# Optimization experiments

Hardware: AMD Instinct MI355X
Metric: run time of the kernel (lower is better)

Reference implementation:

```python
import jax, jax.numpy as jnp
import numpy as np
import math

D = 256
H = 8
HD = D // H
FF = 1024


def pos2posemb(pos, num_pos_feats=64, temperature=10000.0):
    scale = 2 * math.pi
    pos = pos * scale
    dim_t = jnp.arange(num_pos_feats, dtype=jnp.float32)
    dim_t = temperature ** (2.0 * jnp.floor(dim_t / 2) / num_pos_feats)
    pe = pos[..., None] / dim_t  # [N,4,64]
    pe = jnp.stack((jnp.sin(pe[..., 0::2]), jnp.cos(pe[..., 1::2])), axis=-1)  # [N,4,32,2]
    return pe.reshape(pe.shape[0], -1)  # [N,256]


def layer_norm(x, w, b, eps=1e-5):
    m = jnp.mean(x, axis=-1, keepdims=True)
    v = jnp.mean((x - m) ** 2, axis=-1, keepdims=True)
    return (x - m) * jax.lax.rsqrt(v + eps) * w + b


def setup_inputs() -> dict:
    key = jax.random.key(0)
    ks = jax.random.split(key, 24)
    N = 4096
    s = 0.02
    inp = {
        "ref_pts": jax.random.uniform(ks[0], (N, 4), jnp.float32),
        "pred_boxes": jax.random.uniform(ks[1], (N, 4), jnp.float32),
        "scores": jax.random.uniform(ks[2], (N,), jnp.float32),
        "output_embedding": jax.random.normal(ks[3], (N, D), jnp.float32),
        "query_pos": jax.random.normal(ks[4], (N, D), jnp.float32),
        "group_ids": jax.random.randint(ks[5], (N,), 0, 4, jnp.int64),
        "g_size": 4,
        "in_proj_w": jax.random.normal(ks[6], (3 * D, D), jnp.float32) * s,
        "in_proj_b": jnp.zeros((3 * D,), jnp.float32),
        "out_proj_w": jax.random.normal(ks[7], (D, D), jnp.float32) * s,
        "out_proj_b": jnp.zeros((D,), jnp.float32),
        "lin1_w": jax.random.normal(ks[8], (FF, D), jnp.float32) * s,
        "lin1_b": jnp.zeros((FF,), jnp.float32),
        "lin2_w": jax.random.normal(ks[9], (D, FF), jnp.float32) * s,
        "lin2_b": jnp.zeros((D,), jnp.float32),
        "feat1_w": jax.random.normal(ks[10], (FF, D), jnp.float32) * s,
        "feat1_b": jnp.zeros((FF,), jnp.float32),
        "feat2_w": jax.random.normal(ks[11], (D, FF), jnp.float32) * s,
        "feat2_b": jnp.zeros((D,), jnp.float32),
        "norm1_w": jnp.ones((D,), jnp.float32),
        "norm1_b": jnp.zeros((D,), jnp.float32),
        "norm2_w": jnp.ones((D,), jnp.float32),
        "norm2_b": jnp.zeros((D,), jnp.float32),
        "normf_w": jnp.ones((D,), jnp.float32),
        "normf_b": jnp.zeros((D,), jnp.float32),
    }
    return inp


def reference(ref_pts, pred_boxes, scores, output_embedding, query_pos,
              in_proj_w, in_proj_b, out_proj_w, out_proj_b,
              lin1_w, lin1_b, lin2_w, lin2_b,
              feat1_w, feat1_b, feat2_w, feat2_b,
              norm1_w, norm1_b, norm2_w, norm2_b, normf_w, normf_b,
              group_ids, g_size):
    N = ref_pts.shape[0]
    is_pos = scores > 0.5  # score_thr = 0.5
    # ref_pts[is_pos] = pred_boxes.detach()[is_pos]
    ref = jnp.where(is_pos[:, None], jax.lax.stop_gradient(pred_boxes), ref_pts)

    out_embed = output_embedding
    qpos_emb = pos2posemb(ref)  # [N,256]
    qk = qpos_emb + out_embed

    # grouped block-diagonal mask: 0 within same group, -inf across groups
    mask = jnp.where(group_ids[:, None] == group_ids[None, :], 0.0, -jnp.inf)

    # MultiheadAttention (eval, dropout=0)
    q = qk @ in_proj_w[:D].T + in_proj_b[:D]
    k = qk @ in_proj_w[D:2 * D].T + in_proj_b[D:2 * D]
    v = out_embed @ in_proj_w[2 * D:].T + in_proj_b[2 * D:]
    qh = q.reshape(N, H, HD)
    kh = k.reshape(N, H, HD)
    vh = v.reshape(N, H, HD)
    logits = jnp.einsum("nhd,mhd->hnm", qh, kh) / jnp.sqrt(jnp.float32(HD)) + mask
    attn = jax.nn.softmax(logits, axis=-1)
    ctx = jnp.einsum("hnm,mhd->nhd", attn, vh).reshape(N, D)
    tgt2 = ctx @ out_proj_w.T + out_proj_b

    tgt = layer_norm(out_embed + tgt2, norm1_w, norm1_b)
    ffn = jax.nn.relu(tgt @ lin1_w.T + lin1_b) @ lin2_w.T + lin2_b
    tgt = layer_norm(tgt + ffn, norm2_w, norm2_b)

    feat = jax.nn.relu(tgt @ feat1_w.T + feat1_b) @ feat2_w.T + feat2_b
    query_feat = layer_norm(query_pos + feat, normf_w, normf_b)

    # query_pos[is_pos] = query_feat[is_pos]
    query_pos_out = jnp.where(is_pos[:, None], query_feat, query_pos)
    return query_pos_out
```

## Files before the change

kernel.cpp:

```cpp
#include <hip/hip_runtime.h>


typedef __attribute__((ext_vector_type(8))) __bf16 bf16x8;
typedef __attribute__((ext_vector_type(4))) float f32x4;

#define NSPLIT 2

static __device__ __forceinline__ unsigned short f2bf(float f) {
    union { float f; unsigned u; } v; v.f = f;
    unsigned r = v.u + 0x7fffu + ((v.u >> 16) & 1u);
    return (unsigned short)(r >> 16);
}

__global__ __launch_bounds__(1024) void k_setup(
    const float* __restrict__ w0, const float* __restrict__ w1,
    const float* __restrict__ w2, const float* __restrict__ w3,
    const float* __restrict__ w4, const float* __restrict__ w5,
    unsigned short* __restrict__ o0, unsigned short* __restrict__ o1,
    unsigned short* __restrict__ o2, unsigned short* __restrict__ o3,
    unsigned short* __restrict__ o4, unsigned short* __restrict__ o5,
    const int* __restrict__ gid, int N,
    int* __restrict__ perm, int* __restrict__ rank,
    int* __restrict__ gid_s, int* __restrict__ offs)
{
    if (blockIdx.x < 320) {
        long i = ((long)blockIdx.x * 1024 + threadIdx.x) * 4;
        const float* src; unsigned short* dst; long off;
        if      (i <  196608) { src = w0; dst = o0; off = i; }
        else if (i <  262144) { src = w1; dst = o1; off = i -  196608; }
        else if (i <  524288) { src = w2; dst = o2; off = i -  262144; }
        else if (i <  786432) { src = w3; dst = o3; off = i -  524288; }
        else if (i < 1048576) { src = w4; dst = o4; off = i -  786432; }
        else                  { src = w5; dst = o5; off = i - 1048576; }
        float4 v = *(const float4*)(src + off);
        ushort4 o; o.x = f2bf(v.x); o.y = f2bf(v.y); o.z = f2bf(v.z); o.w = f2bf(v.w);
        *(ushort4*)(dst + off) = o;
        return;
    }
    __shared__ int cnt[1024][4];
    __shared__ int base[4];
    int t = threadIdx.x;
    int per = N / 1024;
    int c[4] = {0, 0, 0, 0};
    for (int i = 0; i < per; ++i) c[gid[t * per + i] & 3]++;
    for (int g = 0; g < 4; ++g) cnt[t][g] = c[g];
    __syncthreads();
    for (int off = 1; off < 1024; off <<= 1) {
        int v[4] = {0, 0, 0, 0};
        if (t >= off) for (int g = 0; g < 4; ++g) v[g] = cnt[t - off][g];
        __syncthreads();
        if (t >= off) for (int g = 0; g < 4; ++g) cnt[t][g] += v[g];
        __syncthreads();
    }
    if (t == 0) {
        base[0] = 0;
        base[1] = cnt[1023][0];
        base[2] = base[1] + cnt[1023][1];
        base[3] = base[2] + cnt[1023][2];
        offs[0] = 0; offs[1] = base[1]; offs[2] = base[2]; offs[3] = base[3]; offs[4] = N;
    }
    __syncthreads();
    int run[4];
    for (int g = 0; g < 4; ++g) run[g] = base[g] + (t ? cnt[t - 1][g] : 0);
    for (int i = 0; i < per; ++i) {
        int n = t * per + i;
        int g = gid[n] & 3;
        int p = run[g]++;
        perm[p] = n; rank[n] = p; gid_s[p] = g;
    }
}

__global__ __launch_bounds__(256) void k_prep(
    const float* __restrict__ ref_pts, const float* __restrict__ pred_boxes,
    const float* __restrict__ scores, const float* __restrict__ embed,
    const float* __restrict__ qpos, const int* __restrict__ rank,
    unsigned short* __restrict__ qk_bf, unsigned short* __restrict__ emb_bf,
    float* __restrict__ emb_f32s, float* __restrict__ qpos_s,
    float* __restrict__ scores_s)
{
    int n = blockIdx.x, d = threadIdx.x;
    int pos = rank[n];
    bool ip = scores[n] > 0.5f;
    int c = d >> 6, k = (d >> 1) & 31, s = d & 1;
    float p = (ip ? pred_boxes : ref_pts)[n * 4 + c] * 6.283185307179586f;
    float freq = exp2f(-(float)k * (13.287712379549449f / 32.0f));
    float ang = p * freq;
    float e = s ? cosf(ang) : sinf(ang);
    float em = embed[(size_t)n * 256 + d];
    qk_bf[(size_t)pos * 256 + d] = f2bf(e + em);
    emb_bf[(size_t)pos * 256 + d] = f2bf(em);
    emb_f32s[(size_t)pos * 256 + d] = em;
    qpos_s[(size_t)pos * 256 + d] = qpos[(size_t)n * 256 + d];
    if (d == 0) scores_s[pos] = scores[n];
}

#define EPI_QKV     0
#define EPI_RELUBF  3

template<int EPI>
__global__ __launch_bounds__(256) void k_gemm(
    const unsigned short* __restrict__ A, const unsigned short* __restrict__ A2,
    const unsigned short* __restrict__ B,
    const float* __restrict__ bias,
    void* __restrict__ out, void* __restrict__ out2,
    int M, int Nout, int K)
{
    __shared__ __align__(16) unsigned short As[2][64][72];
    __shared__ __align__(16) unsigned short Bs[2][64][72];
    int mt = M >> 6;
    int bm = blockIdx.x % mt, bn = blockIdx.x / mt;
    int m0 = bm * 64, c0 = bn * 64;
    int tid = threadIdx.x;
    int wave = tid >> 6, lane = tid & 63;
    int wr = wave >> 1, wc = wave & 1;
    int g = lane >> 4, r15 = lane & 15;

    const unsigned short* Asrc = A;
    if constexpr (EPI == EPI_QKV) { if (c0 >= 512) Asrc = A2; }

    int r0 = tid >> 3, u0 = tid & 7;
    int r1 = 32 + (tid >> 3), u1 = tid & 7;

    const unsigned short* Abase = Asrc + (size_t)m0 * K;
    const unsigned short* Bbase = B + (size_t)c0 * K;

    uint4 a0 = *(const uint4*)(Abase + (size_t)r0 * K + u0 * 8);
    uint4 a1 = *(const uint4*)(Abase + (size_t)r1 * K + u1 * 8);
    uint4 b0 = *(const uint4*)(Bbase + (size_t)r0 * K + u0 * 8);
    uint4 b1 = *(const uint4*)(Bbase + (size_t)r1 * K + u1 * 8);
    *(uint4*)(&As[0][r0][u0 * 8]) = a0;
    *(uint4*)(&As[0][r1][u1 * 8]) = a1;
    *(uint4*)(&Bs[0][r0][u0 * 8]) = b0;
    *(uint4*)(&Bs[0][r1][u1 * 8]) = b1;
    __syncthreads();

    f32x4 acc[2][2] = {};
    int nk = K >> 6;
    for (int kt = 0; kt < nk; ++kt) {
        int cur = kt & 1;
        bool more = (kt + 1 < nk);
        if (more) {
            int kc = (kt + 1) << 6;
            a0 = *(const uint4*)(Abase + (size_t)r0 * K + kc + u0 * 8);
            a1 = *(const uint4*)(Abase + (size_t)r1 * K + kc + u1 * 8);
            b0 = *(const uint4*)(Bbase + (size_t)r0 * K + kc + u0 * 8);
            b1 = *(const uint4*)(Bbase + (size_t)r1 * K + kc + u1 * 8);
        }
        #pragma unroll
        for (int kk = 0; kk < 2; ++kk) {
            bf16x8 af0 = *(const bf16x8*)(&As[cur][wr * 32 + r15][kk * 32 + g * 8]);
            bf16x8 af1 = *(const bf16x8*)(&As[cur][wr * 32 + 16 + r15][kk * 32 + g * 8]);
            bf16x8 bf0 = *(const bf16x8*)(&Bs[cur][wc * 32 + r15][kk * 32 + g * 8]);
            bf16x8 bf1 = *(const bf16x8*)(&Bs[cur][wc * 32 + 16 + r15][kk * 32 + g * 8]);
            acc[0][0] = __builtin_amdgcn_mfma_f32_16x16x32_bf16(af0, bf0, acc[0][0], 0, 0, 0);
            acc[0][1] = __builtin_amdgcn_mfma_f32_16x16x32_bf16(af0, bf1, acc[0][1], 0, 0, 0);
            acc[1][0] = __builtin_amdgcn_mfma_f32_16x16x32_bf16(af1, bf0, acc[1][0], 0, 0, 0);
            acc[1][1] = __builtin_amdgcn_mfma_f32_16x16x32_bf16(af1, bf1, acc[1][1], 0, 0, 0);
        }
        if (more) {
            *(uint4*)(&As[cur ^ 1][r0][u0 * 8]) = a0;
            *(uint4*)(&As[cur ^ 1][r1][u1 * 8]) = a1;
            *(uint4*)(&Bs[cur ^ 1][r0][u0 * 8]) = b0;
            *(uint4*)(&Bs[cur ^ 1][r1][u1 * 8]) = b1;
            __syncthreads();
        }
    }

    #pragma unroll
    for (int ti = 0; ti < 2; ++ti)
    #pragma unroll
    for (int tj = 0; tj < 2; ++tj)
    #pragma unroll
    for (int r = 0; r < 4; ++r) {
        int n = m0 + wr * 32 + ti * 16 + g * 4 + r;
        int o = c0 + wc * 32 + tj * 16 + r15;
        float v = acc[ti][tj][r] + bias[o];
        if constexpr (EPI == EPI_QKV) {
            if (o < 512) {
                float s = (o < 256) ? (0.17677669529663687f * 1.4426950408889634f) : 1.0f;
                ((unsigned short*)out)[(size_t)n * 512 + o] = f2bf(v * s);
            } else {
                ((unsigned short*)out2)[(size_t)(o - 512) * M + n] = f2bf(v);
            }
        } else {
            ((unsigned short*)out)[(size_t)n * Nout + o] = f2bf(fmaxf(v, 0.0f));
        }
    }
}

template<int K, int MODE>
__global__ __launch_bounds__(256) void k_gemmln(
    const unsigned short* __restrict__ Abf,
    const float* __restrict__ Opart, const float* __restrict__ lpart,
    const unsigned short* __restrict__ Bw,
    const float* __restrict__ bias, const float* __restrict__ resid,
    const float* __restrict__ lnw, const float* __restrict__ lnb,
    float* __restrict__ outf32, unsigned short* __restrict__ outbf,
    const float* __restrict__ scores_s, const int* __restrict__ perm, int N)
{
    __shared__ __align__(16) unsigned short As[2][16][72];
    __shared__ float sW[4][16];
    __shared__ float qW[4][16];
    __shared__ float mS[16], rS[16];

    const int m0 = blockIdx.x * 16;
    const int tid = threadIdx.x, wave = tid >> 6, lane = tid & 63;
    const int g = lane >> 4, r15 = lane & 15;

    const int ar = tid >> 3, au = tid & 7;
    const bool stager = (tid < 128);

    auto loadA = [&](int kt) -> uint4 {
        int n = m0 + ar;
        int c = kt * 64 + au * 8;
        if constexpr (MODE == 0) {
            int h = c >> 5;
            float l0 = lpart[(size_t)n * 8 + h];
            float l1 = lpart[((size_t)N + n) * 8 + h];
            float inv = 1.0f / (l0 + l1);
            const float* p0 = Opart + (size_t)n * 256 + c;
            const float* p1 = Opart + ((size_t)N + n) * 256 + c;
            float4 x0 = *(const float4*)(p0);
            float4 x1 = *(const float4*)(p0 + 4);
            float4 y0 = *(const float4*)(p1);
            float4 y1 = *(const float4*)(p1 + 4);
            uint4 o;
            o.x = f2bf((x0.x + y0.x) * inv) | ((unsigned)f2bf((x0.y + y0.y) * inv) << 16);
            o.y = f2bf((x0.z + y0.z) * inv) | ((unsigned)f2bf((x0.w + y0.w) * inv) << 16);
            o.z = f2bf((x1.x + y1.x) * inv) | ((unsigned)f2bf((x1.y + y1.y) * inv) << 16);
            o.w = f2bf((x1.z + y1.z) * inv) | ((unsigned)f2bf((x1.w + y1.w) * inv) << 16);
            return o;
        } else {
            return *(const uint4*)(Abf + (size_t)n * K + c);
        }
    };

    const unsigned short* Bb = Bw + (size_t)(wave * 64 + r15) * K + g * 8;
#define LOADB(dst, kt, kk, tj) dst = *(const bf16x8*)(Bb + (size_t)(tj) * 16 * K + (kt) * 64 + (kk) * 32)

    bf16x8 c00, c01, c02, c03, c10, c11, c12, c13;
    uint4 pa;
    if (stager) { pa = loadA(0); *(uint4*)(&As[0][ar][au * 8]) = pa; }
    LOADB(c00, 0, 0, 0); LOADB(c01, 0, 0, 1); LOADB(c02, 0, 0, 2); LOADB(c03, 0, 0, 3);
    LOADB(c10, 0, 1, 0); LOADB(c11, 0, 1, 1); LOADB(c12, 0, 1, 2); LOADB(c13, 0, 1, 3);
    __syncthreads();

    f32x4 acc[4] = {};
    constexpr int nk = K >> 6;
    for (int kt = 0; kt < nk; ++kt) {
        int cur = kt & 1;
        bool more = (kt + 1 < nk);
        bf16x8 n00, n01, n02, n03, n10, n11, n12, n13;
        if (more) {
            if (stager) pa = loadA(kt + 1);
            LOADB(n00, kt + 1, 0, 0); LOADB(n01, kt + 1, 0, 1);
            LOADB(n02, kt + 1, 0, 2); LOADB(n03, kt + 1, 0, 3);
            LOADB(n10, kt + 1, 1, 0); LOADB(n11, kt + 1, 1, 1);
            LOADB(n12, kt + 1, 1, 2); LOADB(n13, kt + 1, 1, 3);
        }
        bf16x8 af0 = *(const bf16x8*)(&As[cur][r15][g * 8]);
        acc[0] = __builtin_amdgcn_mfma_f32_16x16x32_bf16(af0, c00, acc[0], 0, 0, 0);
        acc[1] = __builtin_amdgcn_mfma_f32_16x16x32_bf16(af0, c01, acc[1], 0, 0, 0);
        acc[2] = __builtin_amdgcn_mfma_f32_16x16x32_bf16(af0, c02, acc[2], 0, 0, 0);
        acc[3] = __builtin_amdgcn_mfma_f32_16x16x32_bf16(af0, c03, acc[3], 0, 0, 0);
        bf16x8 af1 = *(const bf16x8*)(&As[cur][r15][32 + g * 8]);
        acc[0] = __builtin_amdgcn_mfma_f32_16x16x32_bf16(af1, c10, acc[0], 0, 0, 0);
        acc[1] = __builtin_amdgcn_mfma_f32_16x16x32_bf16(af1, c11, acc[1], 0, 0, 0);
        acc[2] = __builtin_amdgcn_mfma_f32_16x16x32_bf16(af1, c12, acc[2], 0, 0, 0);
        acc[3] = __builtin_amdgcn_mfma_f32_16x16x32_bf16(af1, c13, acc[3], 0, 0, 0);
        if (more) {
            if (stager) *(uint4*)(&As[cur ^ 1][ar][au * 8]) = pa;
            __syncthreads();
            c00 = n00; c01 = n01; c02 = n02; c03 = n03;
            c10 = n10; c11 = n11; c12 = n12; c13 = n13;
        }
    }
#undef LOADB

    float vals[4][4];
    float vs[4] = {0.f, 0.f, 0.f, 0.f}, vq[4] = {0.f, 0.f, 0.f, 0.f};
    #pragma unroll
    for (int tj = 0; tj < 4; ++tj) {
        int col = wave * 64 + tj * 16 + r15;
        float b = bias[col];
        #pragma unroll
        for (int r = 0; r < 4; ++r) {
            int row = g * 4 + r;
            float v = acc[tj][r] + b + resid[(size_t)(m0 + row) * 256 + col];
            vals[tj][r] = v;
            vs[r] += v; vq[r] += v * v;
        }
    }
    #pragma unroll
    for (int off = 1; off < 16; off <<= 1)
        #pragma unroll
        for (int r = 0; r < 4; ++r) {
            vs[r] += __shfl_xor(vs[r], off, 64);
            vq[r] += __shfl_xor(vq[r], off, 64);
        }
    if (r15 == 0) {
        #pragma unroll
        for (int r = 0; r < 4; ++r) { sW[wave][g * 4 + r] = vs[r]; qW[wave][g * 4 + r] = vq[r]; }
    }
    __syncthreads();
    if (tid < 16) {
        float s = sW[0][tid] + sW[1][tid] + sW[2][tid] + sW[3][tid];
        float q = qW[0][tid] + qW[1][tid] + qW[2][tid] + qW[3][tid];
        float mean = s * (1.0f / 256.0f);
        float var = q * (1.0f / 256.0f) - mean * mean;
        mS[tid] = mean;
        rS[tid] = rsqrtf(fmaxf(var, 0.f) + 1e-5f);
    }
    __syncthreads();

    #pragma unroll
    for (int tj = 0; tj < 4; ++tj) {
        int col = wave * 64 + tj * 16 + r15;
        float w = lnw[col], bb = lnb[col];
        #pragma unroll
        for (int r = 0; r < 4; ++r) {
            int row = g * 4 + r;
            float o = (vals[tj][r] - mS[row]) * rS[row] * w + bb;
            if constexpr (MODE == 0) {
                outf32[(size_t)(m0 + row) * 256 + col] = o;
                outbf[(size_t)(m0 + row) * 256 + col] = f2bf(o);
            } else if constexpr (MODE == 1) {
                outbf[(size_t)(m0 + row) * 256 + col] = f2bf(o);
            } else {
                bool ip = scores_s[m0 + row] > 0.5f;
                float qp = resid[(size_t)(m0 + row) * 256 + col];
                int no = perm[m0 + row];
                outf32[(size_t)no * 256 + col] = ip ? o : qp;
            }
        }
    }
}

__global__ __launch_bounds__(256) void k_attn(
    const unsigned short* __restrict__ QK, const unsigned short* __restrict__ Vt,
    const int* __restrict__ gid_s, const int* __restrict__ offs,
    float* __restrict__ Opart, float* __restrict__ lpart, int N)
{
    __shared__ __align__(16) unsigned short Ks[2][64][40];
    __shared__ __align__(16) unsigned short Vs[2][32][72];
    __shared__ __align__(16) unsigned short Ps[4][16][64];
    __shared__ __align__(16) int gks[2][64];

    int qtiles = N >> 6;
    int bid = blockIdx.x;
    int qt = bid % qtiles;
    int hs = bid / qtiles;
    int h = hs & 7;
    int sp = hs >> 3;
    int q0 = qt * 64;
    int tid = threadIdx.x, wave = tid >> 6, lane = tid & 63;
    int g = lane >> 4, r15 = lane & 15;
    int n0 = q0 + wave * 16;

    int g_lo = gid_s[q0], g_hi = gid_s[q0 + 63];
    int tlo = offs[g_lo] >> 6;
    int thi = (offs[g_hi + 1] + 63) >> 6;
    int ntiles = thi - tlo;
    int chunk = (ntiles + NSPLIT - 1) / NSPLIT;
    int t0 = tlo + sp * chunk;
    int t1 = min(t0 + chunk, thi);

    if (t0 >= t1) {
        #pragma unroll
        for (int r = 0; r < 4; ++r) {
            int n = n0 + g * 4 + r;
            Opart[((size_t)sp * N + n) * 256 + h * 32 + r15] = 0.f;
            Opart[((size_t)sp * N + n) * 256 + h * 32 + 16 + r15] = 0.f;
        }
        if (g == 0) lpart[((size_t)sp * N + n0 + r15) * 8 + h] = 0.f;
        return;
    }

    bf16x8 qf = *(const bf16x8*)(QK + (size_t)(n0 + r15) * 512 + h * 32 + g * 8);
    int gq = gid_s[n0 + r15];

    int kr_ = tid >> 2, kc_ = (tid & 3) * 8;
    int vd_ = tid >> 3, vc_ = (tid & 7) * 8;

    f32x4 O0 = {}, O1 = {};
    float lloc = 0.f;
    unsigned short* PsW = &Ps[wave][0][0];

    {
        int m0 = t0 << 6;
        *(uint4*)(&Ks[0][kr_][kc_]) = *(const uint4*)(QK + (size_t)(m0 + kr_) * 512 + 256 + h * 32 + kc_);
        *(uint4*)(&Vs[0][vd_][vc_]) = *(const uint4*)(Vt + (size_t)(h * 32 + vd_) * N + m0 + vc_);
        if (tid < 64) gks[0][tid] = gid_s[m0 + tid];
    }
    __syncthreads();

    int cur = 0;
    for (int t = t0; t < t1; ++t) {
        bool more = (t + 1 < t1);
        uint4 kn, vn; int gn = 0;
        if (more) {
            int m0n = (t + 1) << 6;
            kn = *(const uint4*)(QK + (size_t)(m0n + kr_) * 512 + 256 + h * 32 + kc_);
            vn = *(const uint4*)(Vt + (size_t)(h * 32 + vd_) * N + m0n + vc_);
            if (tid < 64) gn = gid_s[m0n + tid];
        }

        f32x4 S[4];
        #pragma unroll
        for (int t_ = 0; t_ < 4; ++t_) {
            bf16x8 kf = *(const bf16x8*)(&Ks[cur][t_ * 16 + r15][g * 8]);
            f32x4 z = {};
            S[t_] = __builtin_amdgcn_mfma_f32_16x16x32_bf16(kf, qf, z, 0, 0, 0);
        }
        #pragma unroll
        for (int t_ = 0; t_ < 4; ++t_) {
            int4 g4 = *(const int4*)(&gks[cur][t_ * 16 + g * 4]);
            float p0 = (g4.x == gq) ? exp2f(S[t_][0]) : 0.f;
            float p1 = (g4.y == gq) ? exp2f(S[t_][1]) : 0.f;
            float p2 = (g4.z == gq) ? exp2f(S[t_][2]) : 0.f;
            float p3 = (g4.w == gq) ? exp2f(S[t_][3]) : 0.f;
            lloc += (p0 + p1) + (p2 + p3);
            ushort4 pw;
            pw.x = f2bf(p0); pw.y = f2bf(p1); pw.z = f2bf(p2); pw.w = f2bf(p3);
            int off = t_ * 32 + g * 8;
            int byte = r15 * 128 + ((((off >> 4) ^ (r15 & 7)) << 4) | (off & 15));
            *(ushort4*)((char*)PsW + byte) = pw;
        }
        #pragma unroll
        for (int kk = 0; kk < 2; ++kk) {
            int byte = r15 * 128 + (((kk * 4 + g) ^ (r15 & 7)) << 4);
            bf16x8 pf = *(const bf16x8*)((char*)PsW + byte);
            bf16x8 v0 = *(const bf16x8*)(&Vs[cur][r15][kk * 32 + g * 8]);
            bf16x8 v1 = *(const bf16x8*)(&Vs[cur][16 + r15][kk * 32 + g * 8]);
            O0 = __builtin_amdgcn_mfma_f32_16x16x32_bf16(pf, v0, O0, 0, 0, 0);
            O1 = __builtin_amdgcn_mfma_f32_16x16x32_bf16(pf, v1, O1, 0, 0, 0);
        }

        if (more) {
            *(uint4*)(&Ks[cur ^ 1][kr_][kc_]) = kn;
            *(uint4*)(&Vs[cur ^ 1][vd_][vc_]) = vn;
            if (tid < 64) gks[cur ^ 1][tid] = gn;
        }
        __syncthreads();
        cur ^= 1;
    }

    float l = lloc;
    l += __shfl_xor(l, 16, 64);
    l += __shfl_xor(l, 32, 64);
    if (g == 0) lpart[((size_t)sp * N + n0 + r15) * 8 + h] = l;

    #pragma unroll
    for (int r = 0; r < 4; ++r) {
        int n = n0 + g * 4 + r;
        Opart[((size_t)sp * N + n) * 256 + h * 32 + r15]      = O0[r];
        Opart[((size_t)sp * N + n) * 256 + h * 32 + 16 + r15] = O1[r];
    }
}

extern "C" void kernel_launch(void* const* d_in, const int* in_sizes, int n_in,
                              void* d_out, int out_size, void* d_ws, size_t ws_size,
                              hipStream_t stream)
{
    const float* ref_pts    = (const float*)d_in[0];
    const float* pred_boxes = (const float*)d_in[1];
    const float* scores     = (const float*)d_in[2];
    const float* out_embed  = (const float*)d_in[3];
    const float* query_pos  = (const float*)d_in[4];
    const int*   group_ids  = (const int*)d_in[5];
    const float* in_proj_w  = (const float*)d_in[7];
    const float* in_proj_b  = (const float*)d_in[8];
    const float* out_proj_w = (const float*)d_in[9];
    const float* out_proj_b = (const float*)d_in[10];
    const float* lin1_w     = (const float*)d_in[11];
    const float* lin1_b     = (const float*)d_in[12];
    const float* lin2_w     = (const float*)d_in[13];
    const float* lin2_b     = (const float*)d_in[14];
    const float* feat1_w    = (const float*)d_in[15];
    const float* feat1_b    = (const float*)d_in[16];
    const float* feat2_w    = (const float*)d_in[17];
    const float* feat2_b    = (const float*)d_in[18];
    const float* norm1_w    = (const float*)d_in[19];
    const float* norm1_b    = (const float*)d_in[20];
    const float* norm2_w    = (const float*)d_in[21];
    const float* norm2_b    = (const float*)d_in[22];
    const float* normf_w    = (const float*)d_in[23];
    const float* normf_b    = (const float*)d_in[24];

    const int N = in_sizes[2];

    char* ws = (char*)d_ws;
    size_t off = 0;
    auto alloc = [&](size_t bytes) -> void* {
        void* p = ws + off; off += (bytes + 255) & ~(size_t)255; return p;
    };
    unsigned short* wqkv   = (unsigned short*)alloc((size_t)768 * 256 * 2);
    unsigned short* wout   = (unsigned short*)alloc((size_t)256 * 256 * 2);
    unsigned short* wlin1  = (unsigned short*)alloc((size_t)1024 * 256 * 2);
    unsigned short* wlin2  = (unsigned short*)alloc((size_t)256 * 1024 * 2);
    unsigned short* wfeat1 = (unsigned short*)alloc((size_t)1024 * 256 * 2);
    unsigned short* wfeat2 = (unsigned short*)alloc((size_t)256 * 1024 * 2);
    unsigned short* qk_bf  = (unsigned short*)alloc((size_t)N * 256 * 2);
    unsigned short* emb_bf = (unsigned short*)alloc((size_t)N * 256 * 2);
    unsigned short* QKbuf  = (unsigned short*)alloc((size_t)N * 512 * 2);
    unsigned short* Vtbuf  = (unsigned short*)alloc((size_t)256 * N * 2);
    float*          tgtf   = (float*)alloc((size_t)N * 256 * 4);
    unsigned short* tgtbf  = (unsigned short*)alloc((size_t)N * 256 * 2);
    unsigned short* t2bf   = (unsigned short*)alloc((size_t)N * 256 * 2);
    unsigned short* hbuf   = (unsigned short*)alloc((size_t)N * 1024 * 2);
    float* emb_f32s = (float*)alloc((size_t)N * 256 * 4);
    float* qpos_s   = (float*)alloc((size_t)N * 256 * 4);
    float* scores_s = (float*)alloc((size_t)N * 4);
    int* permbuf = (int*)alloc((size_t)N * 4);
    int* rankbuf = (int*)alloc((size_t)N * 4);
    int* gidsbuf = (int*)alloc((size_t)N * 4);
    int* offsbuf = (int*)alloc(32 * 4);
    float* Opartbuf = (float*)alloc((size_t)NSPLIT * N * 256 * 4);
    float* lbuf     = (float*)alloc((size_t)NSPLIT * N * 8 * 4);
    (void)ws_size; (void)n_in; (void)out_size;

    const int mt = N >> 6;

    k_setup<<<321, 1024, 0, stream>>>(in_proj_w, out_proj_w, lin1_w, lin2_w, feat1_w, feat2_w,
                                      wqkv, wout, wlin1, wlin2, wfeat1, wfeat2,
                                      group_ids, N, permbuf, rankbuf, gidsbuf, offsbuf);
    k_prep<<<N, 256, 0, stream>>>(ref_pts, pred_boxes, scores, out_embed, query_pos, rankbuf,
                                  qk_bf, emb_bf, emb_f32s, qpos_s, scores_s);
    k_gemm<EPI_QKV><<<mt * 12, 256, 0, stream>>>(
        qk_bf, emb_bf, wqkv, in_proj_b, QKbuf, Vtbuf, N, 768, 256);
    k_attn<<<mt * 8 * NSPLIT, 256, 0, stream>>>(QKbuf, Vtbuf, gidsbuf, offsbuf,
                                                Opartbuf, lbuf, N);
    k_gemmln<256, 0><<<N / 16, 256, 0, stream>>>(
        nullptr, Opartbuf, lbuf, wout, out_proj_b, emb_f32s,
        norm1_w, norm1_b, tgtf, tgtbf, nullptr, nullptr, N);
    k_gemm<EPI_RELUBF><<<mt * 16, 256, 0, stream>>>(
        tgtbf, nullptr, wlin1, lin1_b, hbuf, nullptr, N, 1024, 256);
    k_gemmln<1024, 1><<<N / 16, 256, 0, stream>>>(
        hbuf, nullptr, nullptr, wlin2, lin2_b, tgtf,
        norm2_w, norm2_b, nullptr, t2bf, nullptr, nullptr, N);
    k_gemm<EPI_RELUBF><<<mt * 16, 256, 0, stream>>>(
        t2bf, nullptr, wfeat1, feat1_b, hbuf, nullptr, N, 1024, 256);
    k_gemmln<1024, 2><<<N / 16, 256, 0, stream>>>(
        hbuf, nullptr, nullptr, wfeat2, feat2_b, qpos_s,
        normf_w, normf_b, (float*)d_out, nullptr, scores_s, permbuf, N);
}
```

Baseline: 123.4 us.

## Fuse FFN up-projection, ReLU, down-projection and LayerNorm into one kernel

Each of the two FFN stages (lin1/lin2 and feat1/feat2) now runs as a single 512-thread kernel per 16-row tile. It computes the 1024-wide ReLU hidden activation into shared memory, then does the down-projection, residual add and LayerNorm without a global round trip. This removes the N×1024 bf16 hidden buffer write and read-back and two kernel launches per FFN. In exchange, the fused kernel uses 16-row tiles, so each block re-streams the full W1 and W2 weights from cache, and its larger LDS footprint may limit occupancy.

```diff
diff --git a/kernel.cpp b/kernel.cpp
--- a/kernel.cpp
+++ b/kernel.cpp
@@ -94,8 +94,7 @@
     if (d == 0) scores_s[pos] = scores[n];
 }
 
-#define EPI_QKV     0
-#define EPI_RELUBF  3
+#define EPI_QKV 0
 
 template<int EPI>
 __global__ __launch_bounds__(256) void k_gemm(
@@ -175,28 +174,21 @@
         int n = m0 + wr * 32 + ti * 16 + g * 4 + r;
         int o = c0 + wc * 32 + tj * 16 + r15;
         float v = acc[ti][tj][r] + bias[o];
-        if constexpr (EPI == EPI_QKV) {
-            if (o < 512) {
-                float s = (o < 256) ? (0.17677669529663687f * 1.4426950408889634f) : 1.0f;
-                ((unsigned short*)out)[(size_t)n * 512 + o] = f2bf(v * s);
-            } else {
-                ((unsigned short*)out2)[(size_t)(o - 512) * M + n] = f2bf(v);
-            }
+        if (o < 512) {
+            float s = (o < 256) ? (0.17677669529663687f * 1.4426950408889634f) : 1.0f;
+            ((unsigned short*)out)[(size_t)n * 512 + o] = f2bf(v * s);
         } else {
-            ((unsigned short*)out)[(size_t)n * Nout + o] = f2bf(fmaxf(v, 0.0f));
-        }
-    }
-}
-
-template<int K, int MODE>
-__global__ __launch_bounds__(256) void k_gemmln(
-    const unsigned short* __restrict__ Abf,
+            ((unsigned short*)out2)[(size_t)(o - 512) * M + n] = f2bf(v);
+        }
+    }
+}
+
+__global__ __launch_bounds__(256) void k_gemmln0(
     const float* __restrict__ Opart, const float* __restrict__ lpart,
     const unsigned short* __restrict__ Bw,
     const float* __restrict__ bias, const float* __restrict__ resid,
     const float* __restrict__ lnw, const float* __restrict__ lnb,
-    float* __restrict__ outf32, unsigned short* __restrict__ outbf,
-    const float* __restrict__ scores_s, const int* __restrict__ perm, int N)
+    float* __restrict__ outf32, unsigned short* __restrict__ outbf, int N)
 {
     __shared__ __align__(16) unsigned short As[2][16][72];
     __shared__ float sW[4][16];
@@ -206,37 +198,32 @@
     const int m0 = blockIdx.x * 16;
     const int tid = threadIdx.x, wave = tid >> 6, lane = tid & 63;
     const int g = lane >> 4, r15 = lane & 15;
-
     const int ar = tid >> 3, au = tid & 7;
     const bool stager = (tid < 128);
 
     auto loadA = [&](int kt) -> uint4 {
         int n = m0 + ar;
         int c = kt * 64 + au * 8;
-        if constexpr (MODE == 0) {
-            int h = c >> 5;
-            float l0 = lpart[(size_t)n * 8 + h];
-            float l1 = lpart[((size_t)N + n) * 8 + h];
-            float inv = 1.0f / (l0 + l1);
-            const float* p0 = Opart + (size_t)n * 256 + c;
-            const float* p1 = Opart + ((size_t)N + n) * 256 + c;
-            float4 x0 = *(const float4*)(p0);
-            float4 x1 = *(const float4*)(p0 + 4);
-            float4 y0 = *(const float4*)(p1);
-            float4 y1 = *(const float4*)(p1 + 4);
-            uint4 o;
-            o.x = f2bf((x0.x + y0.x) * inv) | ((unsigned)f2bf((x0.y + y0.y) * inv) << 16);
-            o.y = f2bf((x0.z + y0.z) * inv) | ((unsigned)f2bf((x0.w + y0.w) * inv) << 16);
-            o.z = f2bf((x1.x + y1.x) * inv) | ((unsigned)f2bf((x1.y + y1.y) * inv) << 16);
-            o.w = f2bf((x1.z + y1.z) * inv) | ((unsigned)f2bf((x1.w + y1.w) * inv) << 16);
-            return o;
-        } else {
-            return *(const uint4*)(Abf + (size_t)n * K + c);
-        }
+        int h = c >> 5;
+        float l0 = lpart[(size_t)n * 8 + h];
+        float l1 = lpart[((size_t)N + n) * 8 + h];
+        float inv = 1.0f / (l0 + l1);
+        const float* p0 = Opart + (size_t)n * 256 + c;
+        const float* p1 = Opart + ((size_t)N + n) * 256 + c;
+        float4 x0 = *(const float4*)(p0);
+        float4 x1 = *(const float4*)(p0 + 4);
+        float4 y0 = *(const float4*)(p1);
+        float4 y1 = *(const float4*)(p1 + 4);
+        uint4 o;
+        o.x = f2bf((x0.x + y0.x) * inv) | ((unsigned)f2bf((x0.y + y0.y) * inv) << 16);
+        o.y = f2bf((x0.z + y0.z) * inv) | ((unsigned)f2bf((x0.w + y0.w) * inv) << 16);
+        o.z = f2bf((x1.x + y1.x) * inv) | ((unsigned)f2bf((x1.y + y1.y) * inv) << 16);
+        o.w = f2bf((x1.z + y1.z) * inv) | ((unsigned)f2bf((x1.w + y1.w) * inv) << 16);
+        return o;
     };
 
-    const unsigned short* Bb = Bw + (size_t)(wave * 64 + r15) * K + g * 8;
-#define LOADB(dst, kt, kk, tj) dst = *(const bf16x8*)(Bb + (size_t)(tj) * 16 * K + (kt) * 64 + (kk) * 32)
+    const unsigned short* Bb = Bw + (size_t)(wave * 64 + r15) * 256 + g * 8;
+#define LOADB(dst, kt, kk, tj) dst = *(const bf16x8*)(Bb + (size_t)(tj) * 16 * 256 + (kt) * 64 + (kk) * 32)
 
     bf16x8 c00, c01, c02, c03, c10, c11, c12, c13;
     uint4 pa;
@@ -246,10 +233,10 @@
     __syncthreads();
 
     f32x4 acc[4] = {};
-    constexpr int nk = K >> 6;
-    for (int kt = 0; kt < nk; ++kt) {
+    #pragma unroll
+    for (int kt = 0; kt < 4; ++kt) {
         int cur = kt & 1;
-        bool more = (kt + 1 < nk);
+        bool more = (kt + 1 < 4);
         bf16x8 n00, n01, n02, n03, n10, n11, n12, n13;
         if (more) {
             if (stager) pa = loadA(kt + 1);
@@ -321,10 +308,165 @@
         for (int r = 0; r < 4; ++r) {
             int row = g * 4 + r;
             float o = (vals[tj][r] - mS[row]) * rS[row] * w + bb;
-            if constexpr (MODE == 0) {
-                outf32[(size_t)(m0 + row) * 256 + col] = o;
-                outbf[(size_t)(m0 + row) * 256 + col] = f2bf(o);
-            } else if constexpr (MODE == 1) {
+            outf32[(size_t)(m0 + row) * 256 + col] = o;
+            outbf[(size_t)(m0 + row) * 256 + col] = f2bf(o);
+        }
+    }
+}
+
+template<int MODE>
+__global__ __launch_bounds__(512) void k_ffn(
+    const unsigned short* __restrict__ Abf,
+    const unsigned short* __restrict__ W1, const float* __restrict__ b1,
+    const unsigned short* __restrict__ W2, const float* __restrict__ b2,
+    const float* __restrict__ resid,
+    const float* __restrict__ lnw, const float* __restrict__ lnb,
+    float* __restrict__ outf32, unsigned short* __restrict__ outbf,
+    const float* __restrict__ scores_s, const int* __restrict__ perm, int N)
+{
+    __shared__ __align__(16) unsigned short Xs[16][264];
+    __shared__ __align__(16) unsigned short Hs[16][1032];
+    __shared__ float sW[8][16];
+    __shared__ float qW[8][16];
+    __shared__ float mS[16], rS[16];
+
+    const int m0 = blockIdx.x * 16;
+    const int tid = threadIdx.x, wave = tid >> 6, lane = tid & 63;
+    const int g = lane >> 4, r15 = lane & 15;
+
+    {
+        int row = tid >> 5, ch = tid & 31;
+        *(uint4*)(&Xs[row][ch * 8]) = *(const uint4*)(Abf + (size_t)(m0 + row) * 256 + ch * 8);
+    }
+    __syncthreads();
+
+    const unsigned short* B1b = W1 + (size_t)(wave * 128 + r15) * 256 + g * 8;
+#define LB1(dst, ob, kt, kk, tj) \
+    dst = *(const bf16x8*)(B1b + (size_t)((ob) * 64 + (tj) * 16) * 256 + (kt) * 64 + (kk) * 32)
+
+    {
+        bf16x8 bc[8], bn[8];
+        LB1(bc[0], 0, 0, 0, 0); LB1(bc[1], 0, 0, 0, 1); LB1(bc[2], 0, 0, 0, 2); LB1(bc[3], 0, 0, 0, 3);
+        LB1(bc[4], 0, 0, 1, 0); LB1(bc[5], 0, 0, 1, 1); LB1(bc[6], 0, 0, 1, 2); LB1(bc[7], 0, 0, 1, 3);
+        #pragma unroll
+        for (int ob = 0; ob < 2; ++ob) {
+            f32x4 acc[4] = {};
+            #pragma unroll
+            for (int kt = 0; kt < 4; ++kt) {
+                bool more = (ob * 4 + kt + 1 < 8);
+                if (more) {
+                    int s = ob * 4 + kt + 1;
+                    int obn = s >> 2, ktn = s & 3;
+                    LB1(bn[0], obn, ktn, 0, 0); LB1(bn[1], obn, ktn, 0, 1);
+                    LB1(bn[2], obn, ktn, 0, 2); LB1(bn[3], obn, ktn, 0, 3);
+                    LB1(bn[4], obn, ktn, 1, 0); LB1(bn[5], obn, ktn, 1, 1);
+                    LB1(bn[6], obn, ktn, 1, 2); LB1(bn[7], obn, ktn, 1, 3);
+                }
+                bf16x8 a0 = *(const bf16x8*)(&Xs[r15][kt * 64 + g * 8]);
+                acc[0] = __builtin_amdgcn_mfma_f32_16x16x32_bf16(a0, bc[0], acc[0], 0, 0, 0);
+                acc[1] = __builtin_amdgcn_mfma_f32_16x16x32_bf16(a0, bc[1], acc[1], 0, 0, 0);
+                acc[2] = __builtin_amdgcn_mfma_f32_16x16x32_bf16(a0, bc[2], acc[2], 0, 0, 0);
+                acc[3] = __builtin_amdgcn_mfma_f32_16x16x32_bf16(a0, bc[3], acc[3], 0, 0, 0);
+                bf16x8 a1 = *(const bf16x8*)(&Xs[r15][kt * 64 + 32 + g * 8]);
+                acc[0] = __builtin_amdgcn_mfma_f32_16x16x32_bf16(a1, bc[4], acc[0], 0, 0, 0);
+                acc[1] = __builtin_amdgcn_mfma_f32_16x16x32_bf16(a1, bc[5], acc[1], 0, 0, 0);
+                acc[2] = __builtin_amdgcn_mfma_f32_16x16x32_bf16(a1, bc[6], acc[2], 0, 0, 0);
+                acc[3] = __builtin_amdgcn_mfma_f32_16x16x32_bf16(a1, bc[7], acc[3], 0, 0, 0);
+                if (more) {
+                    #pragma unroll
+                    for (int i = 0; i < 8; ++i) bc[i] = bn[i];
+                }
+            }
+            #pragma unroll
+            for (int tj = 0; tj < 4; ++tj) {
+                int col = wave * 128 + ob * 64 + tj * 16 + r15;
+                float b = b1[col];
+                #pragma unroll
+                for (int r = 0; r < 4; ++r) {
+                    Hs[g * 4 + r][col] = f2bf(fmaxf(acc[tj][r] + b, 0.0f));
+                }
+            }
+        }
+    }
+#undef LB1
+    __syncthreads();
+
+    const unsigned short* B2b = W2 + (size_t)(wave * 32 + r15) * 1024 + g * 8;
+#define LB2(dst, kt, kk, tj) \
+    dst = *(const bf16x8*)(B2b + (size_t)(tj) * 16 * 1024 + (kt) * 64 + (kk) * 32)
+
+    f32x4 acc2[2] = {};
+    {
+        bf16x8 bc[4], bn[4];
+        LB2(bc[0], 0, 0, 0); LB2(bc[1], 0, 0, 1);
+        LB2(bc[2], 0, 1, 0); LB2(bc[3], 0, 1, 1);
+        #pragma unroll
+        for (int kt = 0; kt < 16; ++kt) {
+            bool more = (kt + 1 < 16);
+            if (more) {
+                LB2(bn[0], kt + 1, 0, 0); LB2(bn[1], kt + 1, 0, 1);
+                LB2(bn[2], kt + 1, 1, 0); LB2(bn[3], kt + 1, 1, 1);
+            }
+            bf16x8 a0 = *(const bf16x8*)(&Hs[r15][kt * 64 + g * 8]);
+            acc2[0] = __builtin_amdgcn_mfma_f32_16x16x32_bf16(a0, bc[0], acc2[0], 0, 0, 0);
+            acc2[1] = __builtin_amdgcn_mfma_f32_16x16x32_bf16(a0, bc[1], acc2[1], 0, 0, 0);
+            bf16x8 a1 = *(const bf16x8*)(&Hs[r15][kt * 64 + 32 + g * 8]);
+            acc2[0] = __builtin_amdgcn_mfma_f32_16x16x32_bf16(a1, bc[2], acc2[0], 0, 0, 0);
+            acc2[1] = __builtin_amdgcn_mfma_f32_16x16x32_bf16(a1, bc[3], acc2[1], 0, 0, 0);
+            if (more) {
+                #pragma unroll
+                for (int i = 0; i < 4; ++i) bc[i] = bn[i];
+            }
+        }
+    }
+#undef LB2
+
+    float vals[2][4];
+    float vs[4] = {0.f, 0.f, 0.f, 0.f}, vq[4] = {0.f, 0.f, 0.f, 0.f};
+    #pragma unroll
+    for (int tj = 0; tj < 2; ++tj) {
+        int col = wave * 32 + tj * 16 + r15;
+        float b = b2[col];
+        #pragma unroll
+        for (int r = 0; r < 4; ++r) {
+            int row = g * 4 + r;
+            float v = acc2[tj][r] + b + resid[(size_t)(m0 + row) * 256 + col];
+            vals[tj][r] = v;
+            vs[r] += v; vq[r] += v * v;
+        }
+    }
+    #pragma unroll
+    for (int off = 1; off < 16; off <<= 1)
+        #pragma unroll
+        for (int r = 0; r < 4; ++r) {
+            vs[r] += __shfl_xor(vs[r], off, 64);
+            vq[r] += __shfl_xor(vq[r], off, 64);
+        }
+    if (r15 == 0) {
+        #pragma unroll
+        for (int r = 0; r < 4; ++r) { sW[wave][g * 4 + r] = vs[r]; qW[wave][g * 4 + r] = vq[r]; }
+    }
+    __syncthreads();
+    if (tid < 16) {
+        float s = 0.f, q = 0.f;
+        #pragma unroll
+        for (int w = 0; w < 8; ++w) { s += sW[w][tid]; q += qW[w][tid]; }
+        float mean = s * (1.0f / 256.0f);
+        float var = q * (1.0f / 256.0f) - mean * mean;
+        mS[tid] = mean;
+        rS[tid] = rsqrtf(fmaxf(var, 0.f) + 1e-5f);
+    }
+    __syncthreads();
+
+    #pragma unroll
+    for (int tj = 0; tj < 2; ++tj) {
+        int col = wave * 32 + tj * 16 + r15;
+        float w = lnw[col], bb = lnb[col];
+        #pragma unroll
+        for (int r = 0; r < 4; ++r) {
+            int row = g * 4 + r;
+            float o = (vals[tj][r] - mS[row]) * rS[row] * w + bb;
+            if constexpr (MODE == 1) {
                 outbf[(size_t)(m0 + row) * 256 + col] = f2bf(o);
             } else {
                 bool ip = scores_s[m0 + row] > 0.5f;
@@ -507,7 +649,6 @@
     float*          tgtf   = (float*)alloc((size_t)N * 256 * 4);
     unsigned short* tgtbf  = (unsigned short*)alloc((size_t)N * 256 * 2);
     unsigned short* t2bf   = (unsigned short*)alloc((size_t)N * 256 * 2);
-    unsigned short* hbuf   = (unsigned short*)alloc((size_t)N * 1024 * 2);
     float* emb_f32s = (float*)alloc((size_t)N * 256 * 4);
     float* qpos_s   = (float*)alloc((size_t)N * 256 * 4);
     float* scores_s = (float*)alloc((size_t)N * 4);
@@ -530,17 +671,13 @@
         qk_bf, emb_bf, wqkv, in_proj_b, QKbuf, Vtbuf, N, 768, 256);
     k_attn<<<mt * 8 * NSPLIT, 256, 0, stream>>>(QKbuf, Vtbuf, gidsbuf, offsbuf,
                                                 Opartbuf, lbuf, N);
-    k_gemmln<256, 0><<<N / 16, 256, 0, stream>>>(
-        nullptr, Opartbuf, lbuf, wout, out_proj_b, emb_f32s,
-        norm1_w, norm1_b, tgtf, tgtbf, nullptr, nullptr, N);
-    k_gemm<EPI_RELUBF><<<mt * 16, 256, 0, stream>>>(
-        tgtbf, nullptr, wlin1, lin1_b, hbuf, nullptr, N, 1024, 256);
-    k_gemmln<1024, 1><<<N / 16, 256, 0, stream>>>(
-        hbuf, nullptr, nullptr, wlin2, lin2_b, tgtf,
+    k_gemmln0<<<N / 16, 256, 0, stream>>>(
+        Opartbuf, lbuf, wout, out_proj_b, emb_f32s,
+        norm1_w, norm1_b, tgtf, tgtbf, N);
+    k_ffn<1><<<N / 16, 512, 0, stream>>>(
+        tgtbf, wlin1, lin1_b, wlin2, lin2_b, tgtf,
         norm2_w, norm2_b, nullptr, t2bf, nullptr, nullptr, N);
-    k_gemm<EPI_RELUBF><<<mt * 16, 256, 0, stream>>>(
-        t2bf, nullptr, wfeat1, feat1_b, hbuf, nullptr, N, 1024, 256);
-    k_gemmln<1024, 2><<<N / 16, 256, 0, stream>>>(
-        hbuf, nullptr, nullptr, wfeat2, feat2_b, qpos_s,
+    k_ffn<2><<<N / 16, 512, 0, stream>>>(
+        t2bf, wfeat1, feat1_b, wfeat2, feat2_b, qpos_s,
         normf_w, normf_b, (float*)d_out, nullptr, scores_s, permbuf, N);
 }
```

Result: slower. 135.5 us (+9.8%).

## Fuse prep into setup kernel, gather permuted rows in GEMMs, raise attention split

Applied to the files above, without the earlier changes.

Merges the per-row preprocessing into the setup launch, so it runs alongside the weight conversion and sort. Rows are no longer scattered into sorted order; instead the QKV GEMM and the LN epilogues gather through the permutation. This removes the sorted copies of the fp32 embedding, query_pos and scores, along with one kernel launch. Attention split-K goes from 2 to 4 and the merge step loops over the splits, which adds more partial-output traffic. The gemmln K loop is also fully unrolled.

```diff
diff --git a/kernel.cpp b/kernel.cpp
--- a/kernel.cpp
+++ b/kernel.cpp
@@ -4,7 +4,7 @@
 typedef __attribute__((ext_vector_type(8))) __bf16 bf16x8;
 typedef __attribute__((ext_vector_type(4))) float f32x4;
 
-#define NSPLIT 2
+#define NSPLIT 4
 
 static __device__ __forceinline__ unsigned short f2bf(float f) {
     union { float f; unsigned u; } v; v.f = f;
@@ -20,11 +20,14 @@
     unsigned short* __restrict__ o2, unsigned short* __restrict__ o3,
     unsigned short* __restrict__ o4, unsigned short* __restrict__ o5,
     const int* __restrict__ gid, int N,
-    int* __restrict__ perm, int* __restrict__ rank,
-    int* __restrict__ gid_s, int* __restrict__ offs)
+    int* __restrict__ perm, int* __restrict__ gid_s, int* __restrict__ offs,
+    const float* __restrict__ ref_pts, const float* __restrict__ pred_boxes,
+    const float* __restrict__ scores, const float* __restrict__ embed,
+    unsigned short* __restrict__ qk_bf, unsigned short* __restrict__ emb_bf)
 {
-    if (blockIdx.x < 320) {
-        long i = ((long)blockIdx.x * 1024 + threadIdx.x) * 4;
+    int bid = blockIdx.x, tid = threadIdx.x;
+    if (bid < 320) {
+        long i = ((long)bid * 1024 + tid) * 4;
         const float* src; unsigned short* dst; long off;
         if      (i <  196608) { src = w0; dst = o0; off = i; }
         else if (i <  262144) { src = w1; dst = o1; off = i -  196608; }
@@ -37,49 +40,41 @@
         *(ushort4*)(dst + off) = o;
         return;
     }
-    __shared__ int cnt[1024][4];
-    __shared__ int base[4];
-    int t = threadIdx.x;
-    int per = N / 1024;
-    int c[4] = {0, 0, 0, 0};
-    for (int i = 0; i < per; ++i) c[gid[t * per + i] & 3]++;
-    for (int g = 0; g < 4; ++g) cnt[t][g] = c[g];
-    __syncthreads();
-    for (int off = 1; off < 1024; off <<= 1) {
-        int v[4] = {0, 0, 0, 0};
-        if (t >= off) for (int g = 0; g < 4; ++g) v[g] = cnt[t - off][g];
+    if (bid == 320) {
+        __shared__ int cnt[1024][4];
+        __shared__ int base[4];
+        int t = tid;
+        int per = N / 1024;
+        int c[4] = {0, 0, 0, 0};
+        for (int i = 0; i < per; ++i) c[gid[t * per + i] & 3]++;
+        for (int g = 0; g < 4; ++g) cnt[t][g] = c[g];
         __syncthreads();
-        if (t >= off) for (int g = 0; g < 4; ++g) cnt[t][g] += v[g];
+        for (int off = 1; off < 1024; off <<= 1) {
+            int v[4] = {0, 0, 0, 0};
+            if (t >= off) for (int g = 0; g < 4; ++g) v[g] = cnt[t - off][g];
+            __syncthreads();
+            if (t >= off) for (int g = 0; g < 4; ++g) cnt[t][g] += v[g];
+            __syncthreads();
+        }
+        if (t == 0) {
+            base[0] = 0;
+            base[1] = cnt[1023][0];
+            base[2] = base[1] + cnt[1023][1];
+            base[3] = base[2] + cnt[1023][2];
+            offs[0] = 0; offs[1] = base[1]; offs[2] = base[2]; offs[3] = base[3]; offs[4] = N;
+        }
         __syncthreads();
-    }
-    if (t == 0) {
-        base[0] = 0;
-        base[1] = cnt[1023][0];
-        base[2] = base[1] + cnt[1023][1];
-        base[3] = base[2] + cnt[1023][2];
-        offs[0] = 0; offs[1] = base[1]; offs[2] = base[2]; offs[3] = base[3]; offs[4] = N;
-    }
-    __syncthreads();
-    int run[4];
-    for (int g = 0; g < 4; ++g) run[g] = base[g] + (t ? cnt[t - 1][g] : 0);
-    for (int i = 0; i < per; ++i) {
-        int n = t * per + i;
-        int g = gid[n] & 3;
-        int p = run[g]++;
-        perm[p] = n; rank[n] = p; gid_s[p] = g;
-    }
-}
-
-__global__ __launch_bounds__(256) void k_prep(
-    const float* __restrict__ ref_pts, const float* __restrict__ pred_boxes,
-    const float* __restrict__ scores, const float* __restrict__ embed,
-    const float* __restrict__ qpos, const int* __restrict__ rank,
-    unsigned short* __restrict__ qk_bf, unsigned short* __restrict__ emb_bf,
-    float* __restrict__ emb_f32s, float* __restrict__ qpos_s,
-    float* __restrict__ scores_s)
-{
-    int n = blockIdx.x, d = threadIdx.x;
-    int pos = rank[n];
+        int run[4];
+        for (int g = 0; g < 4; ++g) run[g] = base[g] + (t ? cnt[t - 1][g] : 0);
+        for (int i = 0; i < per; ++i) {
+            int n = t * per + i;
+            int g = gid[n] & 3;
+            int p = run[g]++;
+            perm[p] = n; gid_s[p] = g;
+        }
+        return;
+    }
+    int n = (bid - 321) * 4 + (tid >> 8), d = tid & 255;
     bool ip = scores[n] > 0.5f;
     int c = d >> 6, k = (d >> 1) & 31, s = d & 1;
     float p = (ip ? pred_boxes : ref_pts)[n * 4 + c] * 6.283185307179586f;
@@ -87,11 +82,8 @@
     float ang = p * freq;
     float e = s ? cosf(ang) : sinf(ang);
     float em = embed[(size_t)n * 256 + d];
-    qk_bf[(size_t)pos * 256 + d] = f2bf(e + em);
-    emb_bf[(size_t)pos * 256 + d] = f2bf(em);
-    emb_f32s[(size_t)pos * 256 + d] = em;
-    qpos_s[(size_t)pos * 256 + d] = qpos[(size_t)n * 256 + d];
-    if (d == 0) scores_s[pos] = scores[n];
+    qk_bf[(size_t)n * 256 + d] = f2bf(e + em);
+    emb_bf[(size_t)n * 256 + d] = f2bf(em);
 }
 
 #define EPI_QKV     0
@@ -101,7 +93,7 @@
 __global__ __launch_bounds__(256) void k_gemm(
     const unsigned short* __restrict__ A, const unsigned short* __restrict__ A2,
     const unsigned short* __restrict__ B,
-    const float* __restrict__ bias,
+    const float* __restrict__ bias, const int* __restrict__ perm,
     void* __restrict__ out, void* __restrict__ out2,
     int M, int Nout, int K)
 {
@@ -121,11 +113,13 @@
     int r0 = tid >> 3, u0 = tid & 7;
     int r1 = 32 + (tid >> 3), u1 = tid & 7;
 
-    const unsigned short* Abase = Asrc + (size_t)m0 * K;
+    int pr0 = m0 + r0, pr1 = m0 + r1;
+    if constexpr (EPI == EPI_QKV) { pr0 = perm[m0 + r0]; pr1 = perm[m0 + r1]; }
+
     const unsigned short* Bbase = B + (size_t)c0 * K;
 
-    uint4 a0 = *(const uint4*)(Abase + (size_t)r0 * K + u0 * 8);
-    uint4 a1 = *(const uint4*)(Abase + (size_t)r1 * K + u1 * 8);
+    uint4 a0 = *(const uint4*)(Asrc + (size_t)pr0 * K + u0 * 8);
+    uint4 a1 = *(const uint4*)(Asrc + (size_t)pr1 * K + u1 * 8);
     uint4 b0 = *(const uint4*)(Bbase + (size_t)r0 * K + u0 * 8);
     uint4 b1 = *(const uint4*)(Bbase + (size_t)r1 * K + u1 * 8);
     *(uint4*)(&As[0][r0][u0 * 8]) = a0;
@@ -141,8 +135,8 @@
         bool more = (kt + 1 < nk);
         if (more) {
             int kc = (kt + 1) << 6;
-            a0 = *(const uint4*)(Abase + (size_t)r0 * K + kc + u0 * 8);
-            a1 = *(const uint4*)(Abase + (size_t)r1 * K + kc + u1 * 8);
+            a0 = *(const uint4*)(Asrc + (size_t)pr0 * K + kc + u0 * 8);
+            a1 = *(const uint4*)(Asrc + (size_t)pr1 * K + kc + u1 * 8);
             b0 = *(const uint4*)(Bbase + (size_t)r0 * K + kc + u0 * 8);
             b1 = *(const uint4*)(Bbase + (size_t)r1 * K + kc + u1 * 8);
         }
@@ -196,39 +190,46 @@
     const float* __restrict__ bias, const float* __restrict__ resid,
     const float* __restrict__ lnw, const float* __restrict__ lnb,
     float* __restrict__ outf32, unsigned short* __restrict__ outbf,
-    const float* __restrict__ scores_s, const int* __restrict__ perm, int N)
+    const float* __restrict__ scores, const int* __restrict__ perm, int N)
 {
     __shared__ __align__(16) unsigned short As[2][16][72];
     __shared__ float sW[4][16];
     __shared__ float qW[4][16];
     __shared__ float mS[16], rS[16];
+    __shared__ int pm[16];
 
     const int m0 = blockIdx.x * 16;
     const int tid = threadIdx.x, wave = tid >> 6, lane = tid & 63;
     const int g = lane >> 4, r15 = lane & 15;
-
     const int ar = tid >> 3, au = tid & 7;
     const bool stager = (tid < 128);
+
+    if (tid < 16) pm[tid] = (MODE == 1) ? (m0 + tid) : perm[m0 + tid];
 
     auto loadA = [&](int kt) -> uint4 {
         int n = m0 + ar;
         int c = kt * 64 + au * 8;
         if constexpr (MODE == 0) {
             int h = c >> 5;
-            float l0 = lpart[(size_t)n * 8 + h];
-            float l1 = lpart[((size_t)N + n) * 8 + h];
-            float inv = 1.0f / (l0 + l1);
-            const float* p0 = Opart + (size_t)n * 256 + c;
-            const float* p1 = Opart + ((size_t)N + n) * 256 + c;
-            float4 x0 = *(const float4*)(p0);
-            float4 x1 = *(const float4*)(p0 + 4);
-            float4 y0 = *(const float4*)(p1);
-            float4 y1 = *(const float4*)(p1 + 4);
+            float lsum = 0.f;
+            #pragma unroll
+            for (int s = 0; s < NSPLIT; ++s)
+                lsum += lpart[((size_t)s * N + n) * 8 + h];
+            float inv = 1.0f / lsum;
+            float o8[8] = {};
+            #pragma unroll
+            for (int s = 0; s < NSPLIT; ++s) {
+                const float* p = Opart + ((size_t)s * N + n) * 256 + c;
+                float4 x0 = *(const float4*)(p);
+                float4 x1 = *(const float4*)(p + 4);
+                o8[0] += x0.x; o8[1] += x0.y; o8[2] += x0.z; o8[3] += x0.w;
+                o8[4] += x1.x; o8[5] += x1.y; o8[6] += x1.z; o8[7] += x1.w;
+            }
             uint4 o;
-            o.x = f2bf((x0.x + y0.x) * inv) | ((unsigned)f2bf((x0.y + y0.y) * inv) << 16);
-            o.y = f2bf((x0.z + y0.z) * inv) | ((unsigned)f2bf((x0.w + y0.w) * inv) << 16);
-            o.z = f2bf((x1.x + y1.x) * inv) | ((unsigned)f2bf((x1.y + y1.y) * inv) << 16);
-            o.w = f2bf((x1.z + y1.z) * inv) | ((unsigned)f2bf((x1.w + y1.w) * inv) << 16);
+            o.x = f2bf(o8[0] * inv) | ((unsigned)f2bf(o8[1] * inv) << 16);
+            o.y = f2bf(o8[2] * inv) | ((unsigned)f2bf(o8[3] * inv) << 16);
+            o.z = f2bf(o8[4] * inv) | ((unsigned)f2bf(o8[5] * inv) << 16);
+            o.w = f2bf(o8[6] * inv) | ((unsigned)f2bf(o8[7] * inv) << 16);
             return o;
         } else {
             return *(const uint4*)(Abf + (size_t)n * K + c);
@@ -247,6 +248,7 @@
 
     f32x4 acc[4] = {};
     constexpr int nk = K >> 6;
+    #pragma unroll
     for (int kt = 0; kt < nk; ++kt) {
         int cur = kt & 1;
         bool more = (kt + 1 < nk);
@@ -286,7 +288,7 @@
         #pragma unroll
         for (int r = 0; r < 4; ++r) {
             int row = g * 4 + r;
-            float v = acc[tj][r] + b + resid[(size_t)(m0 + row) * 256 + col];
+            float v = acc[tj][r] + b + resid[(size_t)pm[row] * 256 + col];
             vals[tj][r] = v;
             vs[r] += v; vq[r] += v * v;
         }
@@ -327,9 +329,9 @@
             } else if constexpr (MODE == 1) {
                 outbf[(size_t)(m0 + row) * 256 + col] = f2bf(o);
             } else {
-                bool ip = scores_s[m0 + row] > 0.5f;
-                float qp = resid[(size_t)(m0 + row) * 256 + col];
-                int no = perm[m0 + row];
+                int no = pm[row];
+                bool ip = scores[no] > 0.5f;
+                float qp = resid[(size_t)no * 256 + col];
                 outf32[(size_t)no * 256 + col] = ip ? o : qp;
             }
         }
@@ -508,11 +510,7 @@
     unsigned short* tgtbf  = (unsigned short*)alloc((size_t)N * 256 * 2);
     unsigned short* t2bf   = (unsigned short*)alloc((size_t)N * 256 * 2);
     unsigned short* hbuf   = (unsigned short*)alloc((size_t)N * 1024 * 2);
-    float* emb_f32s = (float*)alloc((size_t)N * 256 * 4);
-    float* qpos_s   = (float*)alloc((size_t)N * 256 * 4);
-    float* scores_s = (float*)alloc((size_t)N * 4);
     int* permbuf = (int*)alloc((size_t)N * 4);
-    int* rankbuf = (int*)alloc((size_t)N * 4);
     int* gidsbuf = (int*)alloc((size_t)N * 4);
     int* offsbuf = (int*)alloc(32 * 4);
     float* Opartbuf = (float*)alloc((size_t)NSPLIT * N * 256 * 4);
@@ -521,26 +519,26 @@
 
     const int mt = N >> 6;
 
-    k_setup<<<321, 1024, 0, stream>>>(in_proj_w, out_proj_w, lin1_w, lin2_w, feat1_w, feat2_w,
-                                      wqkv, wout, wlin1, wlin2, wfeat1, wfeat2,
-                                      group_ids, N, permbuf, rankbuf, gidsbuf, offsbuf);
-    k_prep<<<N, 256, 0, stream>>>(ref_pts, pred_boxes, scores, out_embed, query_pos, rankbuf,
-                                  qk_bf, emb_bf, emb_f32s, qpos_s, scores_s);
+    k_setup<<<1345, 1024, 0, stream>>>(in_proj_w, out_proj_w, lin1_w, lin2_w, feat1_w, feat2_w,
+                                       wqkv, wout, wlin1, wlin2, wfeat1, wfeat2,
+                                       group_ids, N, permbuf, gidsbuf, offsbuf,
+                                       ref_pts, pred_boxes, scores, out_embed,
+                                       qk_bf, emb_bf);
     k_gemm<EPI_QKV><<<mt * 12, 256, 0, stream>>>(
-        qk_bf, emb_bf, wqkv, in_proj_b, QKbuf, Vtbuf, N, 768, 256);
+        qk_bf, emb_bf, wqkv, in_proj_b, permbuf, QKbuf, Vtbuf, N, 768, 256);
     k_attn<<<mt * 8 * NSPLIT, 256, 0, stream>>>(QKbuf, Vtbuf, gidsbuf, offsbuf,
                                                 Opartbuf, lbuf, N);
     k_gemmln<256, 0><<<N / 16, 256, 0, stream>>>(
-        nullptr, Opartbuf, lbuf, wout, out_proj_b, emb_f32s,
-        norm1_w, norm1_b, tgtf, tgtbf, nullptr, nullptr, N);
+        nullptr, Opartbuf, lbuf, wout, out_proj_b, out_embed,
+        norm1_w, norm1_b, tgtf, tgtbf, nullptr, permbuf, N);
     k_gemm<EPI_RELUBF><<<mt * 16, 256, 0, stream>>>(
-        tgtbf, nullptr, wlin1, lin1_b, hbuf, nullptr, N, 1024, 256);
+        tgtbf, nullptr, wlin1, lin1_b, nullptr, hbuf, nullptr, N, 1024, 256);
     k_gemmln<1024, 1><<<N / 16, 256, 0, stream>>>(
         hbuf, nullptr, nullptr, wlin2, lin2_b, tgtf,
-        norm2_w, norm2_b, nullptr, t2bf, nullptr, nullptr, N);
+        norm2_w, norm2_b, nullptr, t2bf, nullptr, permbuf, N);
     k_gemm<EPI_RELUBF><<<mt * 16, 256, 0, stream>>>(
-        t2bf, nullptr, wfeat1, feat1_b, hbuf, nullptr, N, 1024, 256);
+        t2bf, nullptr, wfeat1, feat1_b, nullptr, hbuf, nullptr, N, 1024, 256);
     k_gemmln<1024, 2><<<N / 16, 256, 0, stream>>>(
-        hbuf, nullptr, nullptr, wfeat2, feat2_b, qpos_s,
-        normf_w, normf_b, (float*)d_out, nullptr, scores_s, permbuf, N);
+        hbuf, nullptr, nullptr, wfeat2, feat2_b, query_pos,
+        normf_w, normf_b, (float*)d_out, nullptr, scores, permbuf, N);
 }
```

New measurement: 111.2 us. 9.9% less time.
